# Performance work log

Hardware: AMD Instinct MI355X
Metric: run time of the kernel (lower is better)

## Reference

```python
import jax, jax.numpy as jnp
import numpy as np

B, I, H1, H2, E, T = 16384, 512, 256, 128, 8, 2


def setup_inputs() -> dict:
    key = jax.random.key(0)
    ks = jax.random.split(key, 4)
    # Xavier-ish scaling for stability
    x = jax.random.normal(ks[0], (B, I), dtype=jnp.float32)
    W1 = jax.random.normal(ks[1], (E, I, H1), dtype=jnp.float32) / np.sqrt(I)
    b1 = jnp.zeros((E, H1), dtype=jnp.float32)
    W2 = jax.random.normal(ks[2], (E, H1, H2), dtype=jnp.float32) / np.sqrt(H1)
    b2 = jnp.zeros((E, H2), dtype=jnp.float32)
    Wg = jax.random.normal(ks[3], (T, I, E), dtype=jnp.float32) / np.sqrt(I)
    bg = jnp.zeros((T, E), dtype=jnp.float32)
    return {"x": x, "W1": W1, "b1": b1, "W2": W2, "b2": b2, "Wg": Wg, "bg": bg}


def reference(x, W1, b1, W2, b2, Wg, bg):
    # All experts as one grouped GEMM: [E, B, H1]
    h = jax.nn.relu(jnp.einsum('bi,eih->ebh', x, W1) + b1[:, None, :])
    # Last expert layer (lastlayer_reg=True -> act applied): [E, B, H2]
    e_out = jax.nn.relu(jnp.einsum('ebh,eho->ebo', h, W2) + b2[:, None, :])
    # Per-task gates with softmax over experts: [T, B, E]
    gates = jax.nn.softmax(jnp.einsum('bi,tie->tbe', x, Wg) + bg[:, None, :], axis=-1)
    # Gate-weighted combine of expert outputs: [T, B, H2]
    towers = jnp.einsum('tbe,ebo->tbo', gates, e_out)
    return towers
```

## Files before the change

### kernel.cpp

```cpp
#include <hip/hip_runtime.h>
#include <hip/hip_bf16.h>

#define B_  16384
#define I_  512
#define H1_ 256
#define H2_ 128
#define E_  8
#define T_  2

typedef __attribute__((ext_vector_type(8))) short short8;
typedef __attribute__((ext_vector_type(4))) float float4_t;

__device__ inline unsigned short f2bf(float f) {
    union { float f; unsigned u; } v; v.f = f;
    unsigned r = v.u + 0x7FFFu + ((v.u >> 16) & 1u);
    return (unsigned short)(r >> 16);
}
__device__ inline float bf2f(unsigned short u) {
    union { unsigned u; float f; } v; v.u = ((unsigned)u) << 16;
    return v.f;
}

__device__ inline void async_copy16(const unsigned short* g, unsigned short* l) {
    __builtin_amdgcn_global_load_lds(
        (const __attribute__((address_space(1))) void*)g,
        (__attribute__((address_space(3))) void*)l,
        16, 0, 0);
}

__global__ void conv_x_kernel(const float* __restrict__ x, unsigned short* __restrict__ xb) {
    int idx = blockIdx.x * 256 + threadIdx.x;
    size_t base = (size_t)idx * 8;
    float4_t a = *(const float4_t*)(x + base);
    float4_t b = *(const float4_t*)(x + base + 4);
    short8 s;
    s[0] = (short)f2bf(a[0]); s[1] = (short)f2bf(a[1]);
    s[2] = (short)f2bf(a[2]); s[3] = (short)f2bf(a[3]);
    s[4] = (short)f2bf(b[0]); s[5] = (short)f2bf(b[1]);
    s[6] = (short)f2bf(b[2]); s[7] = (short)f2bf(b[3]);
    *(short8*)(xb + base) = s;
}

__global__ void transpose_bf16_kernel(const float* __restrict__ in, unsigned short* __restrict__ out,
                                      int R, int C) {
    __shared__ float tile[32][33];
    int e = blockIdx.z;
    int c0 = blockIdx.x * 32;
    int r0 = blockIdx.y * 32;
    const float* inp = in + (size_t)e * R * C;
    unsigned short* outp = out + (size_t)e * R * C;
    int tx = threadIdx.x, ty = threadIdx.y;
#pragma unroll
    for (int j = 0; j < 32; j += 8)
        tile[ty + j][tx] = inp[(size_t)(r0 + ty + j) * C + c0 + tx];
    __syncthreads();
#pragma unroll
    for (int j = 0; j < 32; j += 8)
        outp[(size_t)(c0 + ty + j) * R + r0 + tx] = f2bf(tile[tx][ty + j]);
}

__global__ void prep_wgt_kernel(const float* __restrict__ wg, unsigned short* __restrict__ wgt) {
    int idx = blockIdx.x * 256 + threadIdx.x;
    int te = idx >> 9;
    int i  = idx & 511;
    int t = te >> 3, e = te & 7;
    wgt[(size_t)te * I_ + i] = f2bf(wg[(size_t)t * I_ * E_ + (size_t)i * E_ + e]);
}

__global__ void gates_kernel(const unsigned short* __restrict__ xb,
                             const unsigned short* __restrict__ wgt,
                             const float* __restrict__ bg,
                             float* __restrict__ gates) {
    int w = threadIdx.x >> 6, lane = threadIdx.x & 63;
    int row0 = (blockIdx.x * 4 + w) * 16;
    int col = lane & 15, quad = lane >> 4;
    float4_t acc = {0.f, 0.f, 0.f, 0.f};
    const unsigned short* aG = xb + (size_t)(row0 + col) * I_ + quad * 8;
    const unsigned short* bG = wgt + (size_t)col * I_ + quad * 8;
#pragma unroll
    for (int k = 0; k < I_; k += 32) {
        short8 a = *(const short8*)(aG + k);
        short8 b = *(const short8*)(bG + k);
        acc = __builtin_amdgcn_mfma_f32_16x16x32_bf16(a, b, acc, 0, 0, 0);
    }
    float bias = bg[col];
#pragma unroll
    for (int p = 0; p < 4; ++p) {
        float v = acc[p] + bias;
        float m = v;
        m = fmaxf(m, __shfl_xor(m, 1));
        m = fmaxf(m, __shfl_xor(m, 2));
        m = fmaxf(m, __shfl_xor(m, 4));
        float ev = __expf(v - m);
        float s = ev;
        s += __shfl_xor(s, 1);
        s += __shfl_xor(s, 2);
        s += __shfl_xor(s, 4);
        gates[(size_t)(row0 + quad * 4 + p) * 16 + col] = ev / s;
    }
}

__global__ void gemm_relu_kernel(const unsigned short* __restrict__ A, size_t aSE,
                                 const unsigned short* __restrict__ Bt, size_t bSE,
                                 const float* __restrict__ bias, int biasSE,
                                 unsigned short* __restrict__ C, size_t cSE,
                                 int K, int lda, int ldb, int ldc) {
    __shared__ unsigned short As[128 * 64];
    __shared__ unsigned short Bs[128 * 64];
    int e = blockIdx.z;
    const unsigned short* Ae = A + (size_t)e * aSE;
    const unsigned short* Be = Bt + (size_t)e * bSE;
    const float* biasE = bias + (size_t)e * biasSE;
    unsigned short* Ce = C + (size_t)e * cSE;
    int m0 = blockIdx.x * 128, n0 = blockIdx.y * 128;
    int t = threadIdx.x, w = t >> 6, lane = t & 63;
    int col = lane & 15, quad = lane >> 4;
    int wm = (w & 1) * 64, wn = (w >> 1) * 64;

    float4_t acc[4][4];
#pragma unroll
    for (int mi = 0; mi < 4; ++mi)
#pragma unroll
        for (int ni = 0; ni < 4; ++ni)
            acc[mi][ni] = (float4_t){0.f, 0.f, 0.f, 0.f};

    int rT = t >> 3;
    int gk = (((t & 7) ^ (rT & 7))) * 8;
    const unsigned short* aG = Ae + (size_t)(m0 + rT) * lda + gk;
    const unsigned short* bG = Be + (size_t)(n0 + rT) * ldb + gk;
    unsigned short* aL = As + (size_t)w * 64 * 8;
    unsigned short* bL = Bs + (size_t)w * 64 * 8;

    for (int k0 = 0; k0 < K; k0 += 64) {
#pragma unroll
        for (int j = 0; j < 4; ++j) {
            async_copy16(aG + (size_t)j * 32 * lda + k0, aL + j * 2048);
            async_copy16(bG + (size_t)j * 32 * ldb + k0, bL + j * 2048);
        }
        __syncthreads();
#pragma unroll
        for (int kk = 0; kk < 64; kk += 32) {
            int q = (kk >> 3) + quad;
            short8 af[4], bf[4];
#pragma unroll
            for (int mi = 0; mi < 4; ++mi) {
                int r = wm + mi * 16 + col;
                af[mi] = *(const short8*)&As[r * 64 + ((q ^ (r & 7)) * 8)];
            }
#pragma unroll
            for (int ni = 0; ni < 4; ++ni) {
                int r = wn + ni * 16 + col;
                bf[ni] = *(const short8*)&Bs[r * 64 + ((q ^ (r & 7)) * 8)];
            }
#pragma unroll
            for (int mi = 0; mi < 4; ++mi)
#pragma unroll
                for (int ni = 0; ni < 4; ++ni)
                    acc[mi][ni] = __builtin_amdgcn_mfma_f32_16x16x32_bf16(af[mi], bf[ni], acc[mi][ni], 0, 0, 0);
        }
        __syncthreads();
    }

#pragma unroll
    for (int ni = 0; ni < 4; ++ni) {
        int c = n0 + wn + ni * 16 + col;
        float bv = biasE[c];
#pragma unroll
        for (int mi = 0; mi < 4; ++mi) {
            int rbase = m0 + wm + mi * 16 + quad * 4;
#pragma unroll
            for (int p = 0; p < 4; ++p) {
                float v = acc[mi][ni][p] + bv;
                v = v > 0.f ? v : 0.f;
                Ce[(size_t)(rbase + p) * ldc + c] = f2bf(v);
            }
        }
    }
}

__global__ void combine_kernel(const unsigned short* __restrict__ eo,
                               const float* __restrict__ gates,
                               float* __restrict__ out) {
    int idx = blockIdx.x * 256 + threadIdx.x;
    int b = idx >> 4;
    int c0 = (idx & 15) * 8;
    float ga[16];
#pragma unroll
    for (int j = 0; j < 16; ++j) ga[j] = gates[(size_t)b * 16 + j];
    float a0[8], a1[8];
#pragma unroll
    for (int j = 0; j < 8; ++j) { a0[j] = 0.f; a1[j] = 0.f; }
#pragma unroll
    for (int e = 0; e < 8; ++e) {
        short8 v = *(const short8*)(eo + ((size_t)e * B_ + b) * H2_ + c0);
        float w0 = ga[e], w1 = ga[8 + e];
#pragma unroll
        for (int j = 0; j < 8; ++j) {
            float f = bf2f((unsigned short)v[j]);
            a0[j] += w0 * f;
            a1[j] += w1 * f;
        }
    }
    float* o0 = out + (size_t)b * H2_ + c0;
    float* o1 = out + (size_t)B_ * H2_ + (size_t)b * H2_ + c0;
    *(float4_t*)o0 = (float4_t){a0[0], a0[1], a0[2], a0[3]};
    *(float4_t*)(o0 + 4) = (float4_t){a0[4], a0[5], a0[6], a0[7]};
    *(float4_t*)o1 = (float4_t){a1[0], a1[1], a1[2], a1[3]};
    *(float4_t*)(o1 + 4) = (float4_t){a1[4], a1[5], a1[6], a1[7]};
}

extern "C" void kernel_launch(void* const* d_in, const int* in_sizes, int n_in,
                              void* d_out, int out_size, void* d_ws, size_t ws_size,
                              hipStream_t stream) {
    const float* x  = (const float*)d_in[0];
    const float* W1 = (const float*)d_in[1];
    const float* b1 = (const float*)d_in[2];
    const float* W2 = (const float*)d_in[3];
    const float* b2 = (const float*)d_in[4];
    const float* Wg = (const float*)d_in[5];
    const float* bg = (const float*)d_in[6];
    float* out = (float*)d_out;

    char* ws = (char*)d_ws;
    unsigned short* xb    = (unsigned short*)(ws);
    unsigned short* w1t   = (unsigned short*)(ws + 16777216);
    unsigned short* w2t   = (unsigned short*)(ws + 18874368);
    unsigned short* wgt   = (unsigned short*)(ws + 19398656);
    float*          gates = (float*)(ws + 19415040);
    unsigned short* h     = (unsigned short*)(ws + 20463616);
    unsigned short* eo    = (unsigned short*)(ws + 87572480);

    conv_x_kernel<<<dim3(B_ * I_ / 8 / 256), 256, 0, stream>>>(x, xb);
    transpose_bf16_kernel<<<dim3(H1_ / 32, I_ / 32, E_), dim3(32, 8), 0, stream>>>(W1, w1t, I_, H1_);
    transpose_bf16_kernel<<<dim3(H2_ / 32, H1_ / 32, E_), dim3(32, 8), 0, stream>>>(W2, w2t, H1_, H2_);
    prep_wgt_kernel<<<dim3(T_ * E_ * I_ / 256), 256, 0, stream>>>(Wg, wgt);

    gates_kernel<<<dim3(B_ / 64), 256, 0, stream>>>(xb, wgt, bg, gates);

    gemm_relu_kernel<<<dim3(B_ / 128, H1_ / 128, E_), 256, 0, stream>>>(
        xb, 0, w1t, (size_t)H1_ * I_, b1, H1_, h, (size_t)B_ * H1_, I_, I_, I_, H1_);

    gemm_relu_kernel<<<dim3(B_ / 128, H2_ / 128, E_), 256, 0, stream>>>(
        h, (size_t)B_ * H1_, w2t, (size_t)H2_ * H1_, b2, H2_, eo, (size_t)B_ * H2_, H1_, H1_, H1_, H2_);

    combine_kernel<<<dim3(B_ * 16 / 256), 256, 0, stream>>>(eo, gates, out);
}
```

Baseline: 174.8 us.

## Fuse second expert GEMM with gated combine, transpose gate layout

Replaces the layer-2 grouped GEMM and the separate combine kernel with one kernel. Each block handles 64 batch rows and loops over all experts, applying bias, ReLU and the gate weighting in registers. This removes the write and re-read of the bf16 expert outputs and one launch. Gates are now stored transposed so each block can load them into shared memory with vector loads. In exchange the new grid has only 256 blocks, each doing serial per-expert work with no double buffering, so occupancy and load/compute overlap may be weaker.

```diff
diff --git a/kernel.cpp b/kernel.cpp
--- a/kernel.cpp
+++ b/kernel.cpp
@@ -15,10 +15,6 @@
     union { float f; unsigned u; } v; v.f = f;
     unsigned r = v.u + 0x7FFFu + ((v.u >> 16) & 1u);
     return (unsigned short)(r >> 16);
-}
-__device__ inline float bf2f(unsigned short u) {
-    union { unsigned u; float f; } v; v.u = ((unsigned)u) << 16;
-    return v.f;
 }
 
 __device__ inline void async_copy16(const unsigned short* g, unsigned short* l) {
@@ -96,7 +92,7 @@
         s += __shfl_xor(s, 1);
         s += __shfl_xor(s, 2);
         s += __shfl_xor(s, 4);
-        gates[(size_t)(row0 + quad * 4 + p) * 16 + col] = ev / s;
+        gates[(size_t)col * B_ + row0 + quad * 4 + p] = ev / s;
     }
 }
 
@@ -178,35 +174,120 @@
     }
 }
 
-__global__ void combine_kernel(const unsigned short* __restrict__ eo,
-                               const float* __restrict__ gates,
-                               float* __restrict__ out) {
-    int idx = blockIdx.x * 256 + threadIdx.x;
-    int b = idx >> 4;
-    int c0 = (idx & 15) * 8;
-    float ga[16];
-#pragma unroll
-    for (int j = 0; j < 16; ++j) ga[j] = gates[(size_t)b * 16 + j];
-    float a0[8], a1[8];
-#pragma unroll
-    for (int j = 0; j < 8; ++j) { a0[j] = 0.f; a1[j] = 0.f; }
-#pragma unroll
-    for (int e = 0; e < 8; ++e) {
-        short8 v = *(const short8*)(eo + ((size_t)e * B_ + b) * H2_ + c0);
-        float w0 = ga[e], w1 = ga[8 + e];
-#pragma unroll
-        for (int j = 0; j < 8; ++j) {
-            float f = bf2f((unsigned short)v[j]);
-            a0[j] += w0 * f;
-            a1[j] += w1 * f;
-        }
-    }
-    float* o0 = out + (size_t)b * H2_ + c0;
-    float* o1 = out + (size_t)B_ * H2_ + (size_t)b * H2_ + c0;
-    *(float4_t*)o0 = (float4_t){a0[0], a0[1], a0[2], a0[3]};
-    *(float4_t*)(o0 + 4) = (float4_t){a0[4], a0[5], a0[6], a0[7]};
-    *(float4_t*)o1 = (float4_t){a1[0], a1[1], a1[2], a1[3]};
-    *(float4_t*)(o1 + 4) = (float4_t){a1[4], a1[5], a1[6], a1[7]};
+__global__ void fused_l2_combine_kernel(const unsigned short* __restrict__ h,
+                                        const unsigned short* __restrict__ w2t,
+                                        const float* __restrict__ b2,
+                                        const float* __restrict__ gates,
+                                        float* __restrict__ out) {
+    __shared__ unsigned short As[64 * 64];
+    __shared__ unsigned short Bs[128 * 64];
+    __shared__ float gL[16 * 64];
+
+    int b0 = blockIdx.x * 64;
+    int t = threadIdx.x, w = t >> 6, lane = t & 63;
+    int col = lane & 15, quad = lane >> 4;
+    int wn = w * 32;
+
+    {
+        int te = t >> 4, i4 = (t & 15) * 4;
+        *(float4_t*)&gL[te * 64 + i4] = *(const float4_t*)&gates[(size_t)te * B_ + b0 + i4];
+    }
+
+    float4_t tw0[4][2], tw1[4][2];
+#pragma unroll
+    for (int mi = 0; mi < 4; ++mi)
+#pragma unroll
+        for (int ni = 0; ni < 2; ++ni) {
+            tw0[mi][ni] = (float4_t){0.f, 0.f, 0.f, 0.f};
+            tw1[mi][ni] = (float4_t){0.f, 0.f, 0.f, 0.f};
+        }
+
+    int rT = t >> 3;
+    int slot = t & 7;
+
+    for (int e = 0; e < E_; ++e) {
+        const unsigned short* hE = h + (size_t)e * B_ * H1_;
+        const unsigned short* w2E = w2t + (size_t)e * H2_ * H1_;
+
+        float4_t acc[4][2];
+#pragma unroll
+        for (int mi = 0; mi < 4; ++mi)
+#pragma unroll
+            for (int ni = 0; ni < 2; ++ni)
+                acc[mi][ni] = (float4_t){0.f, 0.f, 0.f, 0.f};
+
+        for (int k0 = 0; k0 < H1_; k0 += 64) {
+#pragma unroll
+            for (int j = 0; j < 2; ++j) {
+                int row = j * 32 + rT;
+                int gk = (slot ^ (row & 7)) * 8;
+                async_copy16(hE + (size_t)(b0 + row) * H1_ + k0 + gk,
+                             As + j * 2048 + w * 512);
+            }
+#pragma unroll
+            for (int j = 0; j < 4; ++j) {
+                int row = j * 32 + rT;
+                int gk = (slot ^ (row & 7)) * 8;
+                async_copy16(w2E + (size_t)row * H1_ + k0 + gk,
+                             Bs + j * 2048 + w * 512);
+            }
+            __syncthreads();
+#pragma unroll
+            for (int kk = 0; kk < 64; kk += 32) {
+                int q = (kk >> 3) + quad;
+                short8 af[4], bfr[2];
+#pragma unroll
+                for (int mi = 0; mi < 4; ++mi) {
+                    int r = mi * 16 + col;
+                    af[mi] = *(const short8*)&As[r * 64 + ((q ^ (r & 7)) * 8)];
+                }
+#pragma unroll
+                for (int ni = 0; ni < 2; ++ni) {
+                    int r = wn + ni * 16 + col;
+                    bfr[ni] = *(const short8*)&Bs[r * 64 + ((q ^ (r & 7)) * 8)];
+                }
+#pragma unroll
+                for (int mi = 0; mi < 4; ++mi)
+#pragma unroll
+                    for (int ni = 0; ni < 2; ++ni)
+                        acc[mi][ni] = __builtin_amdgcn_mfma_f32_16x16x32_bf16(af[mi], bfr[ni], acc[mi][ni], 0, 0, 0);
+            }
+            __syncthreads();
+        }
+
+        float bv0 = b2[e * H2_ + wn + col];
+        float bv1 = b2[e * H2_ + wn + 16 + col];
+#pragma unroll
+        for (int mi = 0; mi < 4; ++mi) {
+            float4_t g0 = *(const float4_t*)&gL[e * 64 + mi * 16 + quad * 4];
+            float4_t g1 = *(const float4_t*)&gL[(8 + e) * 64 + mi * 16 + quad * 4];
+#pragma unroll
+            for (int ni = 0; ni < 2; ++ni) {
+                float bv = ni == 0 ? bv0 : bv1;
+#pragma unroll
+                for (int p = 0; p < 4; ++p) {
+                    float v = acc[mi][ni][p] + bv;
+                    v = v > 0.f ? v : 0.f;
+                    tw0[mi][ni][p] += g0[p] * v;
+                    tw1[mi][ni][p] += g1[p] * v;
+                }
+            }
+        }
+    }
+
+#pragma unroll
+    for (int mi = 0; mi < 4; ++mi) {
+#pragma unroll
+        for (int ni = 0; ni < 2; ++ni) {
+            int n = wn + ni * 16 + col;
+#pragma unroll
+            for (int p = 0; p < 4; ++p) {
+                int r = b0 + mi * 16 + quad * 4 + p;
+                out[(size_t)r * H2_ + n] = tw0[mi][ni][p];
+                out[(size_t)B_ * H2_ + (size_t)r * H2_ + n] = tw1[mi][ni][p];
+            }
+        }
+    }
 }
 
 extern "C" void kernel_launch(void* const* d_in, const int* in_sizes, int n_in,
@@ -228,7 +309,6 @@
     unsigned short* wgt   = (unsigned short*)(ws + 19398656);
     float*          gates = (float*)(ws + 19415040);
     unsigned short* h     = (unsigned short*)(ws + 20463616);
-    unsigned short* eo    = (unsigned short*)(ws + 87572480);
 
     conv_x_kernel<<<dim3(B_ * I_ / 8 / 256), 256, 0, stream>>>(x, xb);
     transpose_bf16_kernel<<<dim3(H1_ / 32, I_ / 32, E_), dim3(32, 8), 0, stream>>>(W1, w1t, I_, H1_);
@@ -240,8 +320,5 @@
     gemm_relu_kernel<<<dim3(B_ / 128, H1_ / 128, E_), 256, 0, stream>>>(
         xb, 0, w1t, (size_t)H1_ * I_, b1, H1_, h, (size_t)B_ * H1_, I_, I_, I_, H1_);
 
-    gemm_relu_kernel<<<dim3(B_ / 128, H2_ / 128, E_), 256, 0, stream>>>(
-        h, (size_t)B_ * H1_, w2t, (size_t)H2_ * H1_, b2, H2_, eo, (size_t)B_ * H2_, H1_, H1_, H1_, H2_);
-
-    combine_kernel<<<dim3(B_ * 16 / 256), 256, 0, stream>>>(eo, gates, out);
-}
+    fused_l2_combine_kernel<<<dim3(B_ / 64), 256, 0, stream>>>(h, w2t, b2, gates, out);
+}
```

After: 183.7 us. 1.05x slower.
